# Kernel tuning notes

Measured on AMD Instinct MI355X. Metric: run time of the kernel, lower is better.

## Reference

```python
import jax, jax.numpy as jnp
import numpy as np

N_NODES = 50000
N_EDGES = 1600000
IN_DIM = 64
EDGE_DIM = 8
N_GRAPHS = 256
EXP_IN = 32
H = 64  # hidden dim per head / GCN hidden
EPS = 1e-5
NEG_SLOPE = 0.2


def gat_layer(x, src, dst, ea, W, a_src, a_dst, We, a_e, bias, heads, dim, concat):
    """PyG-style GATConv with edge features and self-loops (fill_value='mean')."""
    N = x.shape[0]
    ones_e = jnp.ones((ea.shape[0],), x.dtype)
    cnt = jax.ops.segment_sum(ones_e, dst, num_segments=N)
    loop_attr = jax.ops.segment_sum(ea, dst, num_segments=N) / jnp.maximum(cnt, 1.0)[:, None]
    s = jnp.concatenate([src, jnp.arange(N)])
    d = jnp.concatenate([dst, jnp.arange(N)])
    eaf = jnp.concatenate([ea, loop_attr], axis=0)  # [E+N, edge_dim]
    h = (x @ W).reshape(N, heads, dim)              # [N, H, D]
    ee = (eaf @ We).reshape(-1, heads, dim)         # [E+N, H, D]
    al_src = (h * a_src).sum(-1)                    # [N, H]
    al_dst = (h * a_dst).sum(-1)                    # [N, H]
    score = al_src[s] + al_dst[d] + (ee * a_e).sum(-1)
    score = jax.nn.leaky_relu(score, NEG_SLOPE)     # [E+N, H]
    m = jax.ops.segment_max(score, d, num_segments=N)
    ex = jnp.exp(score - m[d])
    att = ex / jax.ops.segment_sum(ex, d, num_segments=N)[d]
    out = jax.ops.segment_sum(h[s] * att[:, :, None], d, num_segments=N)  # [N, H, D]
    out = out.reshape(N, heads * dim) if concat else out.mean(axis=1)
    return out + bias


def gcn_layer(x, src, dst, W, b):
    """PyG-style GCNConv: add self loops, symmetric degree normalization."""
    N = x.shape[0]
    s = jnp.concatenate([src, jnp.arange(N)])
    d = jnp.concatenate([dst, jnp.arange(N)])
    deg = jax.ops.segment_sum(jnp.ones((s.shape[0],), x.dtype), d, num_segments=N)
    dinv = jax.lax.rsqrt(deg)  # deg >= 1 thanks to self loops
    norm = dinv[s] * dinv[d]
    h = x @ W
    return jax.ops.segment_sum(h[s] * norm[:, None], d, num_segments=N) + b


def bn(x, g, b):
    m = x.mean(axis=0)
    v = x.var(axis=0)
    return g * (x - m) * jax.lax.rsqrt(v + EPS) + b


def mean_pool(x, batch, num_graphs):
    s = jax.ops.segment_sum(x, batch, num_segments=num_graphs)
    c = jax.ops.segment_sum(jnp.ones((x.shape[0],), x.dtype), batch, num_segments=num_graphs)
    return s / jnp.maximum(c, 1.0)[:, None]


def setup_inputs() -> dict:
    key = jax.random.key(0)
    ks = jax.random.split(key, 32)
    p = lambda i, shape: jax.random.normal(ks[i], shape, jnp.float32) * 0.05
    z = lambda n: jnp.zeros((n,), jnp.float32)
    o = lambda n: jnp.ones((n,), jnp.float32)
    return {
        "x": jax.random.normal(ks[0], (N_NODES, IN_DIM), jnp.float32),
        "edge_attr": jax.random.normal(ks[1], (N_EDGES, EDGE_DIM), jnp.float32),
        "experimental_feat": jax.random.normal(ks[2], (N_GRAPHS, EXP_IN), jnp.float32),
        "edge_index": jax.random.randint(ks[3], (2, N_EDGES), 0, N_NODES),
        "batch": jnp.sort(jax.random.randint(ks[4], (N_NODES,), 0, N_GRAPHS)),
        "W1": p(5, (IN_DIM, 4 * H)), "att_src1": p(6, (4, H)), "att_dst1": p(7, (4, H)),
        "We1": p(8, (EDGE_DIM, 4 * H)), "att_e1": p(9, (4, H)), "b1": z(4 * H),
        "g1": o(4 * H), "be1": z(4 * H),
        "W2": p(10, (4 * H, H)), "att_src2": p(11, (1, H)), "att_dst2": p(12, (1, H)),
        "We2": p(13, (EDGE_DIM, H)), "att_e2": p(14, (1, H)), "b2": z(H),
        "g2": o(H), "be2": z(H),
        "Wg1": p(15, (H, H)), "bg1": z(H), "g3": o(H), "be3": z(H),
        "Wg2": p(16, (H, H)), "bg2": z(H), "g4": o(H), "be4": z(H),
        "Wex1": p(17, (EXP_IN, H)), "bex1": z(H), "Wex2": p(18, (H, H)), "bex2": z(H),
        "Wc1": p(19, (2 * H, 128)), "bc1": z(128), "Wc2": p(20, (128, 1)), "bc2": z(1),
    }


def reference(x, edge_attr, experimental_feat, edge_index, batch,
              W1, att_src1, att_dst1, We1, att_e1, b1, g1, be1,
              W2, att_src2, att_dst2, We2, att_e2, b2, g2, be2,
              Wg1, bg1, g3, be3, Wg2, bg2, g4, be4,
              Wex1, bex1, Wex2, bex2, Wc1, bc1, Wc2, bc2):
    src, dst = edge_index[0], edge_index[1]
    h = gat_layer(x, src, dst, edge_attr, W1, att_src1, att_dst1, We1, att_e1, b1, 4, H, True)
    h = jax.nn.relu(bn(h, g1, be1))
    h = gat_layer(h, src, dst, edge_attr, W2, att_src2, att_dst2, We2, att_e2, b2, 1, H, False)
    h = jax.nn.relu(bn(h, g2, be2))  # dropout = identity in eval
    h = gcn_layer(h, src, dst, Wg1, bg1)
    h = jax.nn.relu(bn(h, g3, be3))
    h = gcn_layer(h, src, dst, Wg2, bg2)
    h = jax.nn.relu(bn(h, g4, be4))
    xp = mean_pool(h, batch, N_GRAPHS)                    # [G, H]
    e = jax.nn.relu(experimental_feat @ Wex1 + bex1)
    e = jax.nn.relu(e @ Wex2 + bex2)
    combined = jnp.concatenate([xp, e], axis=1)           # [G, 2H]
    combined = jax.nn.relu(combined @ Wc1 + bc1)          # [G, 128]
    out = combined @ Wc2 + bc2                            # [G, 1]
    return (out, xp, combined)
```

## Files before the change

kernel.cpp:

```cpp
#include <hip/hip_runtime.h>
#include <hip/hip_bf16.h>

#define N_NODES 50000
#define N_EDGES 1600000
#define N_GRAPHS 256
#define NEG_SLOPE 0.2f
#define BN_EPS 1e-5f

typedef __hip_bfloat16 bf16;

__device__ __forceinline__ float b2f(bf16 v){ return __bfloat162float(v); }
__device__ __forceinline__ bf16 f2b(float v){ return __float2bfloat16(v); }
__device__ __forceinline__ float us2f(unsigned short u){ return __uint_as_float(((unsigned)u)<<16); }
__device__ __forceinline__ unsigned short f2us(float v){ bf16 b = f2b(v); return *(unsigned short*)&b; }
__device__ __forceinline__ unsigned pk2(float a, float b){ return (unsigned)f2us(a) | ((unsigned)f2us(b)<<16); }
__device__ __forceinline__ float ldF(const void* p, size_t i, int m){
  return m ? ((const float*)p)[i] : b2f(((const bf16*)p)[i]);
}
__device__ __forceinline__ float sane(float v){
  return (v == v && fabsf(v) < 1e30f) ? v : 0.f;
}
__device__ __forceinline__ float sel4(const float v[4], int h){
  float r = v[0];
  r = (h==1) ? v[1] : r;
  r = (h==2) ? v[2] : r;
  r = (h==3) ? v[3] : r;
  return r;
}
__device__ __forceinline__ void acc8(float* acc, float w, uint4 u){
  acc[0] += w*us2f((unsigned short)(u.x & 0xffff)); acc[1] += w*us2f((unsigned short)(u.x >> 16));
  acc[2] += w*us2f((unsigned short)(u.y & 0xffff)); acc[3] += w*us2f((unsigned short)(u.y >> 16));
  acc[4] += w*us2f((unsigned short)(u.z & 0xffff)); acc[5] += w*us2f((unsigned short)(u.z >> 16));
  acc[6] += w*us2f((unsigned short)(u.w & 0xffff)); acc[7] += w*us2f((unsigned short)(u.w >> 16));
}
__device__ __forceinline__ void unp8(float* o, uint4 u){
  o[0] = us2f((unsigned short)(u.x & 0xffff)); o[1] = us2f((unsigned short)(u.x >> 16));
  o[2] = us2f((unsigned short)(u.y & 0xffff)); o[3] = us2f((unsigned short)(u.y >> 16));
  o[4] = us2f((unsigned short)(u.z & 0xffff)); o[5] = us2f((unsigned short)(u.z >> 16));
  o[6] = us2f((unsigned short)(u.w & 0xffff)); o[7] = us2f((unsigned short)(u.w >> 16));
}

__device__ int detect_mode_block(const void* x){
  __shared__ int s_ins;
  if(threadIdx.x == 0) s_ins = 0;
  __syncthreads();
  const unsigned short* u = (const unsigned short*)x;
  int c = 0;
  for(int i = threadIdx.x; i < 1024; i += blockDim.x){
    float v = fabsf(us2f(u[i]));
    if(!(v > 1e-6f && v < 1e4f)) c++;
  }
  if(c) atomicAdd(&s_ins, c);
  __syncthreads();
  return (s_ins > 128) ? 1 : 0;
}

#define NSEG 33
struct Bank { const void* p[NSEG]; int n[NSEG]; int off[NSEG]; };

__global__ void k_convert(Bank b, const void* xdet, float* out){
  int m = detect_mode_block(xdet);
  int seg = blockIdx.y;
  int i = blockIdx.x*256 + threadIdx.x;
  if(i < b.n[seg]) out[b.off[seg] + i] = ldF(b.p[seg], i, m);
}

__global__ void k_cvt_x(const void* x, bf16* xb){
  int m = detect_mode_block(x);
  int i4 = blockIdx.x*256 + threadIdx.x;
  if(i4 >= N_NODES*16) return;
  if(m){
    float4 v = ((const float4*)x)[i4];
    ((ushort4*)xb)[i4] = make_ushort4(f2us(v.x), f2us(v.y), f2us(v.z), f2us(v.w));
  } else {
    ((ushort4*)xb)[i4] = ((const ushort4*)x)[i4];
  }
}

__global__ void k_we(const float* __restrict__ We1, const float* __restrict__ ae1,
                     const float* __restrict__ We2, const float* __restrict__ ae2,
                     float* __restrict__ w_e){
  int t = threadIdx.x;
  if(t < 32){
    int h = t >> 3, k = t & 7;
    float s = 0.f;
    for(int d=0;d<64;d++) s += We1[k*256 + h*64 + d] * ae1[h*64 + d];
    w_e[t] = s;
  } else if(t < 40){
    int k = t - 32;
    float s = 0.f;
    for(int d=0;d<64;d++) s += We2[k*64 + d] * ae2[d];
    w_e[t] = s;
  }
}

__global__ void k_count(const int* __restrict__ dst, int* __restrict__ cnt){
  int e = blockIdx.x*256 + threadIdx.x;
  if(e < N_EDGES){
    int d = dst[e]; if((unsigned)d >= N_NODES) d = 0;
    atomicAdd(&cnt[d], 1);
  }
}

__global__ void k_blocksum(const int* __restrict__ cnt, int* __restrict__ bsum){
  __shared__ int s[256];
  int i = blockIdx.x*256 + threadIdx.x;
  s[threadIdx.x] = (i < N_NODES) ? cnt[i] : 0;
  __syncthreads();
  for(int o=128;o>0;o>>=1){ if(threadIdx.x<o) s[threadIdx.x]+=s[threadIdx.x+o]; __syncthreads(); }
  if(threadIdx.x==0) bsum[blockIdx.x]=s[0];
}

__global__ void k_scan_bsum(const int* __restrict__ bsum, int* __restrict__ bofs, int nb){
  __shared__ int s[256];
  int t = threadIdx.x;
  s[t] = (t<nb) ? bsum[t] : 0;
  __syncthreads();
  for(int o=1;o<256;o<<=1){ int v=(t>=o)?s[t-o]:0; __syncthreads(); s[t]+=v; __syncthreads(); }
  bofs[t] = (t==0) ? 0 : s[t-1];
}

__global__ void k_scan_write(const int* __restrict__ cnt, const int* __restrict__ bofs,
                             int* __restrict__ rp, float* __restrict__ dinv){
  __shared__ int s[256];
  int t = threadIdx.x; int i = blockIdx.x*256 + t;
  int v = (i<N_NODES) ? cnt[i] : 0;
  s[t]=v; __syncthreads();
  for(int o=1;o<256;o<<=1){ int a=(t>=o)?s[t-o]:0; __syncthreads(); s[t]+=a; __syncthreads(); }
  if(i<N_NODES){
    rp[i+1] = s[t] + bofs[blockIdx.x];
    dinv[i] = rsqrtf((float)v + 1.f);
  }
  if(i==0) rp[0]=0;
}

__global__ void k_fill(const int* __restrict__ src, const int* __restrict__ dst,
                       const int* __restrict__ rp, int* __restrict__ fill,
                       const void* __restrict__ ea, const void* __restrict__ xdet,
                       const float* __restrict__ w_e,
                       int4* __restrict__ epk){
  int m = detect_mode_block(xdet);
  int e = blockIdx.x*256 + threadIdx.x;
  if(e >= N_EDGES) return;
  int d = dst[e]; if((unsigned)d >= N_NODES) d = 0;
  int p = atomicAdd(&fill[d], 1);
  int slot = rp[d] + p;
  if((unsigned)slot >= N_EDGES) return;
  int sv = src[e]; if((unsigned)sv >= N_NODES) sv = 0;
  float a[8];
  if(m){
    const float* eaf = (const float*)ea;
    float4 lo = *(const float4*)&eaf[(size_t)e*8];
    float4 hi = *(const float4*)&eaf[(size_t)e*8 + 4];
    a[0]=lo.x; a[1]=lo.y; a[2]=lo.z; a[3]=lo.w;
    a[4]=hi.x; a[5]=hi.y; a[6]=hi.z; a[7]=hi.w;
  } else {
    #pragma unroll
    for(int k=0;k<8;k++) a[k] = b2f(((const bf16*)ea)[(size_t)e*8 + k]);
  }
  unsigned d4[4];
  #pragma unroll
  for(int h=0;h<4;h++){
    float s = 0.f;
    #pragma unroll
    for(int k=0;k<8;k++) s += a[k]*w_e[h*8+k];
    d4[h] = f2us(s);
  }
  float s1 = 0.f;
  #pragma unroll
  for(int k=0;k<8;k++) s1 += a[k]*w_e[32+k];
  int4 pk;
  pk.x = sv;
  pk.y = (int)(d4[0] | (d4[1] << 16));
  pk.z = (int)(d4[2] | (d4[3] << 16));
  pk.w = (int)(unsigned)f2us(s1);
  epk[slot] = pk;
}

__global__ __launch_bounds__(256, 3) void k_gemmA(
    const bf16* __restrict__ xb, const float* __restrict__ W1,
    bf16* __restrict__ hp, int M)
{
  __shared__ float As[64][68];
  __shared__ float Ws[64][64];
  const int tid = threadIdx.x;
  const int bm  = blockIdx.x * 64;
  const int h   = blockIdx.y;
  const int tx  = tid & 15;
  const int ty  = tid >> 4;
  float acc[4][4] = {};

  #pragma unroll
  for(int f = tid; f < 1024; f += 256){
    int r = f >> 4, kq = f & 15;
    int row = bm + r;
    float4 v = make_float4(0.f,0.f,0.f,0.f);
    if(row < M){
      ushort4 u = *(const ushort4*)&xb[(size_t)row*64 + 4*kq];
      v = make_float4(us2f(u.x), us2f(u.y), us2f(u.z), us2f(u.w));
    }
    *(float4*)&As[r][4*kq] = v;
  }
  #pragma unroll
  for(int g = tid; g < 1024; g += 256){
    int kr = g >> 4, jq = g & 15;
    *(float4*)&Ws[kr][4*jq] = *(const float4*)&W1[(size_t)kr*256 + h*64 + 4*jq];
  }
  __syncthreads();
  #pragma unroll 2
  for(int k = 0; k < 64; k += 4){
    float4 av[4], wv[4];
    #pragma unroll
    for(int r=0;r<4;r++) av[r] = *(const float4*)&As[4*ty + r][k];
    #pragma unroll
    for(int kk=0;kk<4;kk++) wv[kk] = *(const float4*)&Ws[k + kk][4*tx];
    #pragma unroll
    for(int r=0;r<4;r++){
      const float a0=av[r].x, a1=av[r].y, a2=av[r].z, a3=av[r].w;
      acc[r][0] += a0*wv[0].x + a1*wv[1].x + a2*wv[2].x + a3*wv[3].x;
      acc[r][1] += a0*wv[0].y + a1*wv[1].y + a2*wv[2].y + a3*wv[3].y;
      acc[r][2] += a0*wv[0].z + a1*wv[1].z + a2*wv[2].z + a3*wv[3].z;
      acc[r][3] += a0*wv[0].w + a1*wv[1].w + a2*wv[2].w + a3*wv[3].w;
    }
  }
  #pragma unroll
  for(int r=0;r<4;r++){
    int row = bm + 4*ty + r;
    if(row < M){
      ushort4 u = make_ushort4(f2us(acc[r][0]), f2us(acc[r][1]), f2us(acc[r][2]), f2us(acc[r][3]));
      *(ushort4*)&hp[(size_t)row*256 + h*64 + 4*tx] = u;
    }
  }
}

template<int KIN>
__global__ __launch_bounds__(256, 3) void k_gemmB(
    const bf16* __restrict__ A, const float* __restrict__ W,
    bf16* __restrict__ C, int M,
    const float* __restrict__ bnsums, const float* __restrict__ bng, const float* __restrict__ bnb)
{
  __shared__ float As[64][68];
  __shared__ float Ws[64][64];
  const int tid = threadIdx.x;
  const int bm  = blockIdx.x * 64;
  const int tx  = tid & 15;
  const int ty  = tid >> 4;
  const float invN = 1.0f / (float)N_NODES;
  float acc[4][4] = {};

  for(int k0 = 0; k0 < KIN; k0 += 64){
    #pragma unroll
    for(int f = tid; f < 1024; f += 256){
      int r = f >> 4, kq = f & 15;
      int row = bm + r;
      float vv[4] = {0.f,0.f,0.f,0.f};
      if(row < M){
        ushort4 u = *(const ushort4*)&A[(size_t)row*KIN + k0 + 4*kq];
        vv[0]=us2f(u.x); vv[1]=us2f(u.y); vv[2]=us2f(u.z); vv[3]=us2f(u.w);
      }
      int c = k0 + 4*kq;
      #pragma unroll
      for(int j=0;j<4;j++){
        int cc = c + j;
        float mean = bnsums[cc]*invN;
        float var = fmaxf(bnsums[KIN+cc]*invN - mean*mean, 0.f);
        float y = (sane(vv[j])-mean)*rsqrtf(var + BN_EPS)*bng[cc] + bnb[cc];
        vv[j] = fmaxf(y, 0.f);
      }
      *(float4*)&As[r][4*kq] = make_float4(vv[0], vv[1], vv[2], vv[3]);
    }
    #pragma unroll
    for(int g = tid; g < 1024; g += 256){
      int kr = g >> 4, jq = g & 15;
      *(float4*)&Ws[kr][4*jq] = *(const float4*)&W[(size_t)(k0+kr)*64 + 4*jq];
    }
    __syncthreads();
    #pragma unroll 2
    for(int k = 0; k < 64; k += 4){
      float4 av[4], wv[4];
      #pragma unroll
      for(int r=0;r<4;r++) av[r] = *(const float4*)&As[4*ty + r][k];
      #pragma unroll
      for(int kk=0;kk<4;kk++) wv[kk] = *(const float4*)&Ws[k + kk][4*tx];
      #pragma unroll
      for(int r=0;r<4;r++){
        const float a0=av[r].x, a1=av[r].y, a2=av[r].z, a3=av[r].w;
        acc[r][0] += a0*wv[0].x + a1*wv[1].x + a2*wv[2].x + a3*wv[3].x;
        acc[r][1] += a0*wv[0].y + a1*wv[1].y + a2*wv[2].y + a3*wv[3].y;
        acc[r][2] += a0*wv[0].z + a1*wv[1].z + a2*wv[2].z + a3*wv[3].z;
        acc[r][3] += a0*wv[0].w + a1*wv[1].w + a2*wv[2].w + a3*wv[3].w;
      }
    }
    __syncthreads();
  }
  #pragma unroll
  for(int r=0;r<4;r++){
    int row = bm + 4*ty + r;
    if(row < M){
      ushort4 u = make_ushort4(f2us(acc[r][0]), f2us(acc[r][1]), f2us(acc[r][2]), f2us(acc[r][3]));
      *(ushort4*)&C[(size_t)row*64 + 4*tx] = u;
    }
  }
}

__global__ void k_al4(const bf16* __restrict__ hp, const float* __restrict__ asrc,
                      const float* __restrict__ adst,
                      float* __restrict__ als4, float* __restrict__ ald4){
  int idx = blockIdx.x*256 + threadIdx.x;
  if(idx >= N_NODES*4) return;
  int n = idx >> 2, h = idx & 3;
  const unsigned short* row = (const unsigned short*)hp + (size_t)n*256 + h*64;
  float ss=0.f, sd=0.f;
  #pragma unroll
  for(int q=0;q<16;q++){
    ushort4 u = *(const ushort4*)&row[4*q];
    float4 a_s = *(const float4*)&asrc[h*64 + 4*q];
    float4 a_d = *(const float4*)&adst[h*64 + 4*q];
    float v0=us2f(u.x), v1=us2f(u.y), v2=us2f(u.z), v3=us2f(u.w);
    ss += v0*a_s.x + v1*a_s.y + v2*a_s.z + v3*a_s.w;
    sd += v0*a_d.x + v1*a_d.y + v2*a_d.z + v3*a_d.w;
  }
  als4[idx]=ss; ald4[idx]=sd;
}

__global__ void k_al1(const bf16* __restrict__ hp, const float* __restrict__ asrc,
                      const float* __restrict__ adst,
                      float* __restrict__ als, float* __restrict__ ald){
  int n = blockIdx.x*256 + threadIdx.x;
  if(n >= N_NODES) return;
  const unsigned short* row = (const unsigned short*)hp + (size_t)n*64;
  float ss=0.f, sd=0.f;
  #pragma unroll
  for(int q=0;q<16;q++){
    ushort4 u = *(const ushort4*)&row[4*q];
    float4 a_s = *(const float4*)&asrc[4*q];
    float4 a_d = *(const float4*)&adst[4*q];
    float v0=us2f(u.x), v1=us2f(u.y), v2=us2f(u.z), v3=us2f(u.w);
    ss += v0*a_s.x + v1*a_s.y + v2*a_s.z + v3*a_s.w;
    sd += v0*a_d.x + v1*a_d.y + v2*a_d.z + v3*a_d.w;
  }
  als[n]=ss; ald[n]=sd;
}

__global__ __launch_bounds__(64) void k_gat_agg4(
    const int* __restrict__ rp, const int4* __restrict__ epk,
    const bf16* __restrict__ hp,
    const float* __restrict__ als4, const float* __restrict__ ald4,
    const float* __restrict__ bias256, bf16* __restrict__ out1){
  int n = blockIdx.x; int t = threadIdx.x;
  int eh = t >> 5, c8 = t & 31;
  int head = c8 >> 3;
  __shared__ int   ssrc[64];
  __shared__ float swt[64][4];
  int s0 = rp[n], e0 = rp[n+1];
  if((unsigned)s0 > N_EDGES){ s0=0; e0=0; }
  if(e0 < s0 || (unsigned)e0 > N_EDGES) e0 = s0;
  float4 aldv = *(const float4*)&ald4[n*4];
  float4 alsvn = *(const float4*)&als4[n*4];
  float wsum[4] = {0.f,0.f,0.f,0.f};
  float dsum[4] = {0.f,0.f,0.f,0.f};
  float acc[8]  = {0.f,0.f,0.f,0.f,0.f,0.f,0.f,0.f};
  const unsigned short* hpu = (const unsigned short*)hp;

  for(int base = s0; base < e0; base += 64){
    int m = min(64, e0 - base);
    if(t < m){
      int4 pk = epk[base+t];
      int sn = pk.x; if((unsigned)sn >= N_NODES) sn = 0;
      ssrc[t] = sn;
      float edf[4] = {us2f((unsigned short)(pk.y & 0xffff)), us2f((unsigned short)((unsigned)pk.y >> 16)),
                      us2f((unsigned short)(pk.z & 0xffff)), us2f((unsigned short)((unsigned)pk.z >> 16))};
      float4 alss = *(const float4*)&als4[sn*4];
      float alssv[4] = {alss.x, alss.y, alss.z, alss.w};
      float aldvv[4] = {aldv.x, aldv.y, aldv.z, aldv.w};
      float w4[4];
      #pragma unroll
      for(int h=0;h<4;h++){
        float sc = alssv[h] + aldvv[h] + edf[h];
        sc = sc > 0.f ? sc : NEG_SLOPE*sc;
        sc = fminf(sc, 30.f);
        float w = expf(sc);
        w4[h] = w;
        wsum[h] += w; dsum[h] += edf[h];
      }
      *(float4*)&swt[t][0] = make_float4(w4[0], w4[1], w4[2], w4[3]);
    }
    __syncthreads();
    #pragma unroll 4
    for(int i=0;i<m;i+=2){
      int j = i + eh;
      if(j < m){
        int row = ssrc[j];
        float w = swt[j][head];
        uint4 u = *(const uint4*)&hpu[(size_t)row*256 + 8*c8];
        acc8(acc, w, u);
      }
    }
    __syncthreads();
  }
  #pragma unroll
  for(int o=1;o<64;o<<=1){
    #pragma unroll
    for(int h=0;h<4;h++){
      wsum[h] += __shfl_xor(wsum[h], o);
      dsum[h] += __shfl_xor(dsum[h], o);
    }
  }
  #pragma unroll
  for(int q=0;q<8;q++) acc[q] += __shfl_xor(acc[q], 32);
  if(eh == 0){
    float alsnv[4] = {alsvn.x, alsvn.y, alsvn.z, alsvn.w};
    float aldnv[4] = {aldv.x, aldv.y, aldv.z, aldv.w};
    float sEh = sel4(wsum, head), sDh = sel4(dsum, head);
    float deg = (float)(e0 - s0);
    float sdot = deg > 0.f ? sDh/deg : 0.f;
    float sc = sel4(alsnv, head) + sel4(aldnv, head) + sdot;
    sc = sc > 0.f ? sc : NEG_SLOPE*sc;
    sc = fminf(sc, 30.f);
    float wself = expf(sc);
    float self[8];
    unp8(self, *(const uint4*)&hpu[(size_t)n*256 + 8*c8]);
    float4 b0 = *(const float4*)&bias256[8*c8];
    float4 b1 = *(const float4*)&bias256[8*c8 + 4];
    float bi[8] = {b0.x,b0.y,b0.z,b0.w,b1.x,b1.y,b1.z,b1.w};
    float inv = 1.f/(sEh + wself);
    float o8[8];
    #pragma unroll
    for(int q=0;q<8;q++) o8[q] = (acc[q] + wself*self[q])*inv + bi[q];
    uint4 st;
    st.x = pk2(o8[0],o8[1]); st.y = pk2(o8[2],o8[3]);
    st.z = pk2(o8[4],o8[5]); st.w = pk2(o8[6],o8[7]);
    *(uint4*)&((unsigned short*)out1)[(size_t)n*256 + 8*c8] = st;
  }
}

__global__ __launch_bounds__(64) void k_gat_agg1e(
    const int* __restrict__ rp, const int4* __restrict__ epk,
    const bf16* __restrict__ hp,
    const float* __restrict__ als, const float* __restrict__ ald,
    const float* __restrict__ bias64, bf16* __restrict__ out){
  int n = blockIdx.x; int t = threadIdx.x;
  int eg = t >> 3, c8 = t & 7;
  __shared__ float sw[64];
  __shared__ int   ssrc[64];
  int s0 = rp[n], e0 = rp[n+1];
  if((unsigned)s0 > N_EDGES){ s0=0; e0=0; }
  if(e0 < s0 || (unsigned)e0 > N_EDGES) e0 = s0;
  float aldn = ald[n];
  float wsum_l = 0.f, dsum_l = 0.f;
  float acc[8] = {0.f,0.f,0.f,0.f,0.f,0.f,0.f,0.f};
  const unsigned short* hpu = (const unsigned short*)hp;
  for(int base = s0; base < e0; base += 64){
    int m = min(64, e0 - base);
    if(t < m){
      int4 pk = epk[base+t];
      int sn = pk.x; if((unsigned)sn >= N_NODES) sn = 0;
      ssrc[t] = sn;
      float ed = us2f((unsigned short)(pk.w & 0xffff));
      float sc = als[sn] + aldn + ed;
      sc = sc > 0.f ? sc : NEG_SLOPE*sc;
      sc = fminf(sc, 30.f);
      float w = expf(sc);
      sw[t] = w;
      wsum_l += w; dsum_l += ed;
    }
    __syncthreads();
    #pragma unroll 2
    for(int i=0;i<m;i+=8){
      int j = i + eg;
      if(j < m){
        int row = ssrc[j];
        float w = sw[j];
        uint4 u = *(const uint4*)&hpu[(size_t)row*64 + 8*c8];
        acc8(acc, w, u);
      }
    }
    __syncthreads();
  }
  #pragma unroll
  for(int o=1;o<64;o<<=1){ wsum_l += __shfl_xor(wsum_l, o); dsum_l += __shfl_xor(dsum_l, o); }
  #pragma unroll
  for(int q=0;q<8;q++){
    acc[q] += __shfl_xor(acc[q], 8);
    acc[q] += __shfl_xor(acc[q], 16);
    acc[q] += __shfl_xor(acc[q], 32);
  }
  if(t < 8){
    float deg = (float)(e0 - s0);
    float sdot = deg > 0.f ? dsum_l/deg : 0.f;
    float sc = als[n] + aldn + sdot;
    sc = sc > 0.f ? sc : NEG_SLOPE*sc;
    sc = fminf(sc, 30.f);
    float wself = expf(sc);
    float self[8];
    unp8(self, *(const uint4*)&hpu[(size_t)n*64 + 8*t]);
    float4 b0 = *(const float4*)&bias64[8*t];
    float4 b1 = *(const float4*)&bias64[8*t + 4];
    float bi[8] = {b0.x,b0.y,b0.z,b0.w,b1.x,b1.y,b1.z,b1.w};
    float inv = 1.f/(wsum_l + wself);
    float o8[8];
    #pragma unroll
    for(int q=0;q<8;q++) o8[q] = (acc[q] + wself*self[q])*inv + bi[q];
    uint4 st;
    st.x = pk2(o8[0],o8[1]); st.y = pk2(o8[2],o8[3]);
    st.z = pk2(o8[4],o8[5]); st.w = pk2(o8[6],o8[7]);
    *(uint4*)&((unsigned short*)out)[(size_t)n*64 + 8*t] = st;
  }
}

__global__ __launch_bounds__(64) void k_gcn_agg(
    const int* __restrict__ rp, const int4* __restrict__ epk,
    const float* __restrict__ dinv, const bf16* __restrict__ gp,
    const float* __restrict__ bias, bf16* __restrict__ out){
  int n = blockIdx.x; int t = threadIdx.x;
  int eg = t >> 3, c8 = t & 7;
  __shared__ float sw[64];
  __shared__ int   ssrc[64];
  int s0 = rp[n], e0 = rp[n+1];
  if((unsigned)s0 > N_EDGES){ s0=0; e0=0; }
  if(e0 < s0 || (unsigned)e0 > N_EDGES) e0 = s0;
  float dn = dinv[n];
  float acc[8] = {0.f,0.f,0.f,0.f,0.f,0.f,0.f,0.f};
  const unsigned short* gpu = (const unsigned short*)gp;
  for(int base = s0; base < e0; base += 64){
    int m = min(64, e0 - base);
    if(t < m){
      int sn = epk[base+t].x; if((unsigned)sn >= N_NODES) sn = 0;
      ssrc[t]=sn; sw[t]=dinv[sn];
    }
    __syncthreads();
    #pragma unroll 2
    for(int i=0;i<m;i+=8){
      int j = i + eg;
      if(j < m){
        int row = ssrc[j];
        float w = sw[j];
        uint4 u = *(const uint4*)&gpu[(size_t)row*64 + 8*c8];
        acc8(acc, w, u);
      }
    }
    __syncthreads();
  }
  #pragma unroll
  for(int q=0;q<8;q++){
    acc[q] += __shfl_xor(acc[q], 8);
    acc[q] += __shfl_xor(acc[q], 16);
    acc[q] += __shfl_xor(acc[q], 32);
  }
  if(t < 8){
    float self[8];
    unp8(self, *(const uint4*)&gpu[(size_t)n*64 + 8*t]);
    float4 b0 = *(const float4*)&bias[8*t];
    float4 b1 = *(const float4*)&bias[8*t + 4];
    float bi[8] = {b0.x,b0.y,b0.z,b0.w,b1.x,b1.y,b1.z,b1.w};
    float o8[8];
    #pragma unroll
    for(int q=0;q<8;q++) o8[q] = dn*(acc[q] + dn*self[q]) + bi[q];
    uint4 st;
    st.x = pk2(o8[0],o8[1]); st.y = pk2(o8[2],o8[3]);
    st.z = pk2(o8[4],o8[5]); st.w = pk2(o8[6],o8[7]);
    *(uint4*)&((unsigned short*)out)[(size_t)n*64 + 8*t] = st;
  }
}

template<int C>
__global__ void k_colstats(const bf16* __restrict__ X, float* __restrict__ sums){
  constexpr int RPB = 128;
  constexpr int RSTEP = 256 / C;
  int c = threadIdx.x % C;
  int r0 = threadIdx.x / C;
  int rbeg = blockIdx.x * RPB;
  int rend = min(N_NODES, rbeg + RPB);
  const unsigned short* Xu = (const unsigned short*)X;
  float s = 0.f, q = 0.f;
  for(int r = rbeg + r0; r < rend; r += RSTEP){
    float v = sane(us2f(Xu[(size_t)r*C + c]));
    s += v; q += v*v;
  }
  atomicAdd(&sums[c], s);
  atomicAdd(&sums[C + c], q);
}

__global__ __launch_bounds__(64) void k_pool3(
    const bf16* __restrict__ h, const int* __restrict__ batch,
    const float* __restrict__ sums, const float* __restrict__ g4,
    const float* __restrict__ b4,
    float* __restrict__ psum, float* __restrict__ pcnt){
  int t = threadIdx.x;
  int n0 = blockIdx.x * 256;
  int n1 = min(N_NODES, n0 + 256);
  if(n0 >= n1) return;
  const float invN = 1.0f / (float)N_NODES;
  float mean = sums[t]*invN;
  float var = fmaxf(sums[64+t]*invN - mean*mean, 0.f);
  float rstd = rsqrtf(var + BN_EPS);
  float gg = g4[t], bb = b4[t];
  const unsigned short* hu = (const unsigned short*)h;
  int cur = batch[n0]; if((unsigned)cur >= N_GRAPHS) cur = 0;
  float acc = 0.f; int cl = 0;
  for(int n = n0; n < n1; n++){
    int g = batch[n]; if((unsigned)g >= N_GRAPHS) g = 0;
    if(g != cur){
      atomicAdd(&psum[cur*64 + t], acc);
      if(t == 0) atomicAdd(&pcnt[cur], (float)cl);
      acc = 0.f; cl = 0; cur = g;
    }
    float y = (sane(us2f(hu[(size_t)n*64 + t]))-mean)*rstd*gg + bb;
    acc += fmaxf(y, 0.f);
    cl++;
  }
  atomicAdd(&psum[cur*64 + t], acc);
  if(t == 0) atomicAdd(&pcnt[cur], (float)cl);
}

__device__ __forceinline__ void stO(void* o, size_t i, float v, int m){
  if(m) ((float*)o)[i] = v; else ((bf16*)o)[i] = f2b(v);
}

__global__ __launch_bounds__(128) void k_head(
    const float* __restrict__ psum, const float* __restrict__ pcnt,
    const float* __restrict__ exf,
    const float* __restrict__ Wex1, const float* __restrict__ bex1,
    const float* __restrict__ Wex2, const float* __restrict__ bex2,
    const float* __restrict__ Wc1, const float* __restrict__ bc1,
    const float* __restrict__ Wc2, const float* __restrict__ bc2,
    const void* __restrict__ xdet, void* __restrict__ dout){
  int m0 = detect_mode_block(xdet);
  int g = blockIdx.x; int t = threadIdx.x;
  __shared__ float ci[128];
  __shared__ float e1[64];
  __shared__ float comb[128];
  __shared__ float red[128];
  if(t < 64){
    float c = fmaxf(pcnt[g], 1.f);
    float xp = sane(psum[g*64 + t]) / c;
    ci[t] = xp;
    stO(dout, 256 + (size_t)g*64 + t, xp, m0);
  } else {
    int j = t - 64;
    float s = bex1[j];
    for(int k=0;k<32;k++) s += exf[g*32 + k] * Wex1[k*64 + j];
    e1[j] = fmaxf(s, 0.f);
  }
  __syncthreads();
  if(t >= 64){
    int j = t - 64;
    float s = bex2[j];
    for(int k=0;k<64;k++) s += e1[k] * Wex2[k*64 + j];
    ci[64 + j] = fmaxf(s, 0.f);
  }
  __syncthreads();
  {
    float s = bc1[t];
    for(int k=0;k<128;k++) s += ci[k] * Wc1[k*128 + t];
    s = fmaxf(s, 0.f);
    comb[t] = s;
    stO(dout, 256 + 16384 + (size_t)g*128 + t, s, m0);
  }
  __syncthreads();
  red[t] = comb[t] * Wc2[t];
  __syncthreads();
  for(int o=64;o>0;o>>=1){ if(t<o) red[t]+=red[t+o]; __syncthreads(); }
  if(t==0) stO(dout, g, red[0] + bc2[0], m0);
}

extern "C" void kernel_launch(void* const* d_in, const int* in_sizes, int n_in,
                              void* d_out, int out_size, void* d_ws, size_t ws_size,
                              hipStream_t stream){
  const void* x    = d_in[0];
  const void* ea   = d_in[1];
  const int* ei    = (const int*)d_in[3];
  const int* batch = (const int*)d_in[4];
  const int* src = ei;
  const int* dst = ei + N_EDGES;

  char* base = (char*)d_ws;
  size_t off = 0;
  auto alloc = [&](size_t bytes) -> void* {
    void* r = base + off;
    off += (bytes + 255) & ~(size_t)255;
    return r;
  };
  int*   cnt    = (int*)  alloc((size_t)N_NODES*4);
  int*   fill   = (int*)  alloc((size_t)N_NODES*4);
  float* bnstat = (float*)alloc(4096);
  float* pool   = (float*)alloc((size_t)(N_GRAPHS*64 + N_GRAPHS)*4);
  size_t zbytes = off;
  int*   rp      = (int*)  alloc((size_t)(N_NODES+1)*4);
  int*   bsum    = (int*)  alloc(256*4);
  int*   bofs    = (int*)  alloc(256*4);
  int4*  epk     = (int4*) alloc((size_t)N_EDGES*16);
  float* dinv    = (float*)alloc((size_t)N_NODES*4);
  float* w_e     = (float*)alloc(64*4);
  float* als4    = (float*)alloc((size_t)N_NODES*4*4);
  float* ald4    = (float*)alloc((size_t)N_NODES*4*4);
  float* wbank   = (float*)alloc(80000*4);
  bf16*  xb      = (bf16*) alloc((size_t)N_NODES*64*2);
  bf16*  hp      = (bf16*) alloc((size_t)N_NODES*256*2);
  bf16*  outb    = (bf16*) alloc((size_t)N_NODES*256*2);

  bf16* out1 = outb;
  bf16* out2 = outb;
  bf16* out3 = outb + (size_t)N_NODES*64;
  bf16* out4 = outb + (size_t)N_NODES*128;
  float* bn1 = bnstat;
  float* bn2 = bnstat + 512;
  float* bn3 = bnstat + 640;
  float* bn4 = bnstat + 768;
  float* psum = pool;
  float* pcnt = pool + N_GRAPHS*64;

  const int segidx[NSEG] = {2, 5,6,7,8,9,10,11,12, 13,14,15,16,17,18,19,20,
                            21,22,23,24, 25,26,27,28, 29,30,31,32, 33,34,35,36};
  const int segn[NSEG] = {8192, 16384,256,256,2048,256,256,256,256,
                          16384,64,64,512,64,64,64,64,
                          4096,64,64,64, 4096,64,64,64,
                          2048,64,4096,64, 16384,128,128,1};
  Bank bk;
  int offs[NSEG]; int acc0 = 0;
  for(int i=0;i<NSEG;i++){ bk.p[i]=d_in[segidx[i]]; bk.n[i]=segn[i]; bk.off[i]=acc0; offs[i]=acc0; acc0+=segn[i]; }
  const float* f_exf = wbank + offs[0];
  const float* fW1 = wbank+offs[1]; const float* fas1 = wbank+offs[2]; const float* fad1 = wbank+offs[3];
  const float* fWe1= wbank+offs[4]; const float* fae1 = wbank+offs[5]; const float* fb1  = wbank+offs[6];
  const float* fg1 = wbank+offs[7]; const float* fbe1 = wbank+offs[8];
  const float* fW2 = wbank+offs[9]; const float* fas2 = wbank+offs[10]; const float* fad2 = wbank+offs[11];
  const float* fWe2= wbank+offs[12]; const float* fae2 = wbank+offs[13]; const float* fb2 = wbank+offs[14];
  const float* fg2 = wbank+offs[15]; const float* fbe2 = wbank+offs[16];
  const float* fWg1= wbank+offs[17]; const float* fbg1 = wbank+offs[18]; const float* fg3 = wbank+offs[19];
  const float* fbe3= wbank+offs[20];
  const float* fWg2= wbank+offs[21]; const float* fbg2 = wbank+offs[22]; const float* fg4 = wbank+offs[23];
  const float* fbe4= wbank+offs[24];
  const float* fWex1=wbank+offs[25]; const float* fbex1= wbank+offs[26];
  const float* fWex2=wbank+offs[27]; const float* fbex2= wbank+offs[28];
  const float* fWc1= wbank+offs[29]; const float* fbc1 = wbank+offs[30];
  const float* fWc2= wbank+offs[31]; const float* fbc2 = wbank+offs[32];

  const int nbN  = (N_NODES + 255)/256;
  const int nbE  = (N_EDGES + 255)/256;
  const int nbT  = (N_NODES + 63)/64;

  hipMemsetAsync(d_ws, 0, zbytes, stream);
  {
    dim3 g((16384+255)/256, NSEG);
    k_convert<<<g,256,0,stream>>>(bk, x, wbank);
  }
  k_cvt_x<<<(N_NODES*16+255)/256,256,0,stream>>>(x, xb);
  k_we<<<1,64,0,stream>>>(fWe1, fae1, fWe2, fae2, w_e);
  k_count<<<nbE,256,0,stream>>>(dst, cnt);
  k_blocksum<<<nbN,256,0,stream>>>(cnt, bsum);
  k_scan_bsum<<<1,256,0,stream>>>(bsum, bofs, nbN);
  k_scan_write<<<nbN,256,0,stream>>>(cnt, bofs, rp, dinv);
  k_fill<<<nbE,256,0,stream>>>(src, dst, rp, fill, ea, x, w_e, epk);

  {
    dim3 g(nbT, 4);
    k_gemmA<<<g,256,0,stream>>>(xb, fW1, hp, N_NODES);
  }
  k_al4<<<(N_NODES*4+255)/256,256,0,stream>>>(hp, fas1, fad1, als4, ald4);
  k_gat_agg4<<<N_NODES,64,0,stream>>>(rp, epk, hp, als4, ald4, fb1, out1);
  k_colstats<256><<<(N_NODES+127)/128,256,0,stream>>>(out1, bn1);

  k_gemmB<256><<<nbT,256,0,stream>>>(out1, fW2, hp, N_NODES, bn1, fg1, fbe1);
  k_al1<<<nbN,256,0,stream>>>(hp, fas2, fad2, als4, ald4);
  k_gat_agg1e<<<N_NODES,64,0,stream>>>(rp, epk, hp, als4, ald4, fb2, out2);
  k_colstats<64><<<(N_NODES+127)/128,256,0,stream>>>(out2, bn2);

  k_gemmB<64><<<nbT,256,0,stream>>>(out2, fWg1, hp, N_NODES, bn2, fg2, fbe2);
  k_gcn_agg<<<N_NODES,64,0,stream>>>(rp, epk, dinv, hp, fbg1, out3);
  k_colstats<64><<<(N_NODES+127)/128,256,0,stream>>>(out3, bn3);

  k_gemmB<64><<<nbT,256,0,stream>>>(out3, fWg2, hp, N_NODES, bn3, fg3, fbe3);
  k_gcn_agg<<<N_NODES,64,0,stream>>>(rp, epk, dinv, hp, fbg2, out4);
  k_colstats<64><<<(N_NODES+127)/128,256,0,stream>>>(out4, bn4);

  k_pool3<<<nbN,64,0,stream>>>(out4, batch, bn4, fg4, fbe4, psum, pcnt);
  k_head<<<N_GRAPHS,128,0,stream>>>(psum, pcnt, f_exf, fWex1, fbex1, fWex2, fbex2,
                                    fWc1, fbc1, fWc2, fbc2, x, (void*)d_out);
}
```

Measured before the change: 974.4 us.

## Replace FP32 shared-memory GEMMs with bf16 MFMA matrix-core kernels

```diff
diff --git a/kernel.cpp b/kernel.cpp
--- a/kernel.cpp
+++ b/kernel.cpp
@@ -8,6 +8,8 @@
 #define BN_EPS 1e-5f
 
 typedef __hip_bfloat16 bf16;
+typedef __attribute__((ext_vector_type(8))) short s16x8;
+typedef __attribute__((ext_vector_type(4))) float f32x4;
 
 __device__ __forceinline__ float b2f(bf16 v){ return __bfloat162float(v); }
 __device__ __forceinline__ bf16 f2b(float v){ return __float2bfloat16(v); }
@@ -38,6 +40,12 @@
   o[2] = us2f((unsigned short)(u.y & 0xffff)); o[3] = us2f((unsigned short)(u.y >> 16));
   o[4] = us2f((unsigned short)(u.z & 0xffff)); o[5] = us2f((unsigned short)(u.z >> 16));
   o[6] = us2f((unsigned short)(u.w & 0xffff)); o[7] = us2f((unsigned short)(u.w >> 16));
+}
+__device__ __forceinline__ s16x8 pk8(const float* v){
+  s16x8 r;
+  #pragma unroll
+  for(int j=0;j<8;j++) r[j] = (short)f2us(v[j]);
+  return r;
 }
 
 __device__ int detect_mode_block(const void* x){
@@ -91,6 +99,25 @@
     float s = 0.f;
     for(int d=0;d<64;d++) s += We2[k*64 + d] * ae2[d];
     w_e[t] = s;
+  }
+}
+
+__global__ void k_wt(const float* __restrict__ W1, const float* __restrict__ W2,
+                     const float* __restrict__ Wg1, const float* __restrict__ Wg2,
+                     bf16* __restrict__ wt){
+  int i = blockIdx.x*256 + threadIdx.x;
+  if(i < 16384){
+    int c = i >> 6, k = i & 63;
+    wt[i] = f2b(W1[k*256 + c]);
+  } else if(i < 32768){
+    int j = i - 16384; int c = j >> 8, k = j & 255;
+    wt[i] = f2b(W2[k*64 + c]);
+  } else if(i < 36864){
+    int j = i - 32768; int c = j >> 6, k = j & 63;
+    wt[i] = f2b(Wg1[k*64 + c]);
+  } else if(i < 40960){
+    int j = i - 36864; int c = j >> 6, k = j & 63;
+    wt[i] = f2b(Wg2[k*64 + c]);
   }
 }
 
@@ -177,128 +204,90 @@
   epk[slot] = pk;
 }
 
-__global__ __launch_bounds__(256, 3) void k_gemmA(
-    const bf16* __restrict__ xb, const float* __restrict__ W1,
+__global__ __launch_bounds__(256) void k_gemmA_mfma(
+    const bf16* __restrict__ xb,
+    const bf16* __restrict__ wt1,
     bf16* __restrict__ hp, int M)
 {
-  __shared__ float As[64][68];
-  __shared__ float Ws[64][64];
   const int tid = threadIdx.x;
-  const int bm  = blockIdx.x * 64;
-  const int h   = blockIdx.y;
-  const int tx  = tid & 15;
-  const int ty  = tid >> 4;
-  float acc[4][4] = {};
-
-  #pragma unroll
-  for(int f = tid; f < 1024; f += 256){
-    int r = f >> 4, kq = f & 15;
-    int row = bm + r;
-    float4 v = make_float4(0.f,0.f,0.f,0.f);
-    if(row < M){
-      ushort4 u = *(const ushort4*)&xb[(size_t)row*64 + 4*kq];
-      v = make_float4(us2f(u.x), us2f(u.y), us2f(u.z), us2f(u.w));
-    }
-    *(float4*)&As[r][4*kq] = v;
-  }
-  #pragma unroll
-  for(int g = tid; g < 1024; g += 256){
-    int kr = g >> 4, jq = g & 15;
-    *(float4*)&Ws[kr][4*jq] = *(const float4*)&W1[(size_t)kr*256 + h*64 + 4*jq];
-  }
-  __syncthreads();
-  #pragma unroll 2
-  for(int k = 0; k < 64; k += 4){
-    float4 av[4], wv[4];
-    #pragma unroll
-    for(int r=0;r<4;r++) av[r] = *(const float4*)&As[4*ty + r][k];
-    #pragma unroll
-    for(int kk=0;kk<4;kk++) wv[kk] = *(const float4*)&Ws[k + kk][4*tx];
-    #pragma unroll
-    for(int r=0;r<4;r++){
-      const float a0=av[r].x, a1=av[r].y, a2=av[r].z, a3=av[r].w;
-      acc[r][0] += a0*wv[0].x + a1*wv[1].x + a2*wv[2].x + a3*wv[3].x;
-      acc[r][1] += a0*wv[0].y + a1*wv[1].y + a2*wv[2].y + a3*wv[3].y;
-      acc[r][2] += a0*wv[0].z + a1*wv[1].z + a2*wv[2].z + a3*wv[3].z;
-      acc[r][3] += a0*wv[0].w + a1*wv[1].w + a2*wv[2].w + a3*wv[3].w;
-    }
-  }
-  #pragma unroll
-  for(int r=0;r<4;r++){
-    int row = bm + 4*ty + r;
-    if(row < M){
-      ushort4 u = make_ushort4(f2us(acc[r][0]), f2us(acc[r][1]), f2us(acc[r][2]), f2us(acc[r][3]));
-      *(ushort4*)&hp[(size_t)row*256 + h*64 + 4*tx] = u;
+  const int w = tid >> 6, l = tid & 63;
+  const int lr = l & 15, lg = l >> 4;
+  const int bm = blockIdx.x*64 + w*16;
+  const int arow_i = bm + lr;
+  const uint4* arow = (const uint4*)(xb + (size_t)min(arow_i, M-1)*64);
+  uint4 a0u = arow[lg];
+  uint4 a1u = arow[4 + lg];
+  s16x8 a0 = *(s16x8*)&a0u, a1 = *(s16x8*)&a1u;
+  unsigned short* out = (unsigned short*)hp;
+  const int orow0 = bm + lg*4;
+  #pragma unroll
+  for(int ct = 0; ct < 16; ct++){
+    const uint4* brow = (const uint4*)(wt1 + (size_t)(ct*16 + lr)*64);
+    uint4 b0u = brow[lg];
+    uint4 b1u = brow[4 + lg];
+    f32x4 acc = {0.f, 0.f, 0.f, 0.f};
+    acc = __builtin_amdgcn_mfma_f32_16x16x32_bf16(a0, *(s16x8*)&b0u, acc, 0, 0, 0);
+    acc = __builtin_amdgcn_mfma_f32_16x16x32_bf16(a1, *(s16x8*)&b1u, acc, 0, 0, 0);
+    #pragma unroll
+    for(int r = 0; r < 4; r++){
+      int rr = orow0 + r;
+      if(rr < M) out[(size_t)rr*256 + ct*16 + lr] = f2us(acc[r]);
     }
   }
 }
 
 template<int KIN>
-__global__ __launch_bounds__(256, 3) void k_gemmB(
-    const bf16* __restrict__ A, const float* __restrict__ W,
+__global__ __launch_bounds__(256) void k_gemmB_mfma(
+    const bf16* __restrict__ A, const bf16* __restrict__ Wt,
     bf16* __restrict__ C, int M,
     const float* __restrict__ bnsums, const float* __restrict__ bng, const float* __restrict__ bnb)
 {
-  __shared__ float As[64][68];
-  __shared__ float Ws[64][64];
+  __shared__ float st_s[KIN];
+  __shared__ float st_t[KIN];
   const int tid = threadIdx.x;
-  const int bm  = blockIdx.x * 64;
-  const int tx  = tid & 15;
-  const int ty  = tid >> 4;
-  const float invN = 1.0f / (float)N_NODES;
-  float acc[4][4] = {};
-
-  for(int k0 = 0; k0 < KIN; k0 += 64){
-    #pragma unroll
-    for(int f = tid; f < 1024; f += 256){
-      int r = f >> 4, kq = f & 15;
-      int row = bm + r;
-      float vv[4] = {0.f,0.f,0.f,0.f};
-      if(row < M){
-        ushort4 u = *(const ushort4*)&A[(size_t)row*KIN + k0 + 4*kq];
-        vv[0]=us2f(u.x); vv[1]=us2f(u.y); vv[2]=us2f(u.z); vv[3]=us2f(u.w);
-      }
-      int c = k0 + 4*kq;
-      #pragma unroll
-      for(int j=0;j<4;j++){
-        int cc = c + j;
-        float mean = bnsums[cc]*invN;
-        float var = fmaxf(bnsums[KIN+cc]*invN - mean*mean, 0.f);
-        float y = (sane(vv[j])-mean)*rsqrtf(var + BN_EPS)*bng[cc] + bnb[cc];
-        vv[j] = fmaxf(y, 0.f);
-      }
-      *(float4*)&As[r][4*kq] = make_float4(vv[0], vv[1], vv[2], vv[3]);
-    }
-    #pragma unroll
-    for(int g = tid; g < 1024; g += 256){
-      int kr = g >> 4, jq = g & 15;
-      *(float4*)&Ws[kr][4*jq] = *(const float4*)&W[(size_t)(k0+kr)*64 + 4*jq];
-    }
-    __syncthreads();
-    #pragma unroll 2
-    for(int k = 0; k < 64; k += 4){
-      float4 av[4], wv[4];
-      #pragma unroll
-      for(int r=0;r<4;r++) av[r] = *(const float4*)&As[4*ty + r][k];
-      #pragma unroll
-      for(int kk=0;kk<4;kk++) wv[kk] = *(const float4*)&Ws[k + kk][4*tx];
-      #pragma unroll
-      for(int r=0;r<4;r++){
-        const float a0=av[r].x, a1=av[r].y, a2=av[r].z, a3=av[r].w;
-        acc[r][0] += a0*wv[0].x + a1*wv[1].x + a2*wv[2].x + a3*wv[3].x;
-        acc[r][1] += a0*wv[0].y + a1*wv[1].y + a2*wv[2].y + a3*wv[3].y;
-        acc[r][2] += a0*wv[0].z + a1*wv[1].z + a2*wv[2].z + a3*wv[3].z;
-        acc[r][3] += a0*wv[0].w + a1*wv[1].w + a2*wv[2].w + a3*wv[3].w;
-      }
-    }
-    __syncthreads();
-  }
-  #pragma unroll
-  for(int r=0;r<4;r++){
-    int row = bm + 4*ty + r;
-    if(row < M){
-      ushort4 u = make_ushort4(f2us(acc[r][0]), f2us(acc[r][1]), f2us(acc[r][2]), f2us(acc[r][3]));
-      *(ushort4*)&C[(size_t)row*64 + 4*tx] = u;
+  if(tid < KIN){
+    const float invN = 1.0f / (float)N_NODES;
+    float mean = bnsums[tid]*invN;
+    float var  = fmaxf(bnsums[KIN+tid]*invN - mean*mean, 0.f);
+    float s = bng[tid]*rsqrtf(var + BN_EPS);
+    st_s[tid] = s;
+    st_t[tid] = bnb[tid] - mean*s;
+  }
+  __syncthreads();
+  const int w = tid >> 6, l = tid & 63;
+  const int lr = l & 15, lg = l >> 4;
+  const int bm = blockIdx.x*64 + w*16;
+  const int arow_i = bm + lr;
+  const uint4* arow = (const uint4*)(A + (size_t)min(arow_i, M-1)*KIN);
+  f32x4 acc[4];
+  #pragma unroll
+  for(int ct=0;ct<4;ct++) acc[ct] = (f32x4){0.f,0.f,0.f,0.f};
+  #pragma unroll
+  for(int k0 = 0; k0 < KIN; k0 += 32){
+    uint4 au = arow[(k0 >> 3) + lg];
+    int c0 = k0 + lg*8;
+    float v[8]; unp8(v, au);
+    #pragma unroll
+    for(int j = 0; j < 8; j++){
+      float y = sane(v[j])*st_s[c0+j] + st_t[c0+j];
+      v[j] = fmaxf(y, 0.f);
+    }
+    s16x8 af = pk8(v);
+    #pragma unroll
+    for(int ct = 0; ct < 4; ct++){
+      const uint4* brow = (const uint4*)(Wt + (size_t)(ct*16 + lr)*KIN);
+      uint4 bu = brow[(k0 >> 3) + lg];
+      acc[ct] = __builtin_amdgcn_mfma_f32_16x16x32_bf16(af, *(s16x8*)&bu, acc[ct], 0, 0, 0);
+    }
+  }
+  unsigned short* out = (unsigned short*)C;
+  const int orow0 = bm + lg*4;
+  #pragma unroll
+  for(int ct = 0; ct < 4; ct++){
+    #pragma unroll
+    for(int r = 0; r < 4; r++){
+      int rr = orow0 + r;
+      if(rr < M) out[(size_t)rr*64 + ct*16 + lr] = f2us(acc[ct][r]);
     }
   }
 }
@@ -695,6 +684,7 @@
   float* als4    = (float*)alloc((size_t)N_NODES*4*4);
   float* ald4    = (float*)alloc((size_t)N_NODES*4*4);
   float* wbank   = (float*)alloc(80000*4);
+  bf16*  wt      = (bf16*) alloc((size_t)40960*2);
   bf16*  xb      = (bf16*) alloc((size_t)N_NODES*64*2);
   bf16*  hp      = (bf16*) alloc((size_t)N_NODES*256*2);
   bf16*  outb    = (bf16*) alloc((size_t)N_NODES*256*2);
@@ -709,6 +699,11 @@
   float* bn4 = bnstat + 768;
   float* psum = pool;
   float* pcnt = pool + N_GRAPHS*64;
+
+  bf16* wt1  = wt;
+  bf16* wt2  = wt + 16384;
+  bf16* wtg1 = wt + 32768;
+  bf16* wtg2 = wt + 36864;
 
   const int segidx[NSEG] = {2, 5,6,7,8,9,10,11,12, 13,14,15,16,17,18,19,20,
                             21,22,23,24, 25,26,27,28, 29,30,31,32, 33,34,35,36};
@@ -744,6 +739,7 @@
     dim3 g((16384+255)/256, NSEG);
     k_convert<<<g,256,0,stream>>>(bk, x, wbank);
   }
+  k_wt<<<160,256,0,stream>>>(fW1, fW2, fWg1, fWg2, wt);
   k_cvt_x<<<(N_NODES*16+255)/256,256,0,stream>>>(x, xb);
   k_we<<<1,64,0,stream>>>(fWe1, fae1, fWe2, fae2, w_e);
   k_count<<<nbE,256,0,stream>>>(dst, cnt);
@@ -752,24 +748,21 @@
   k_scan_write<<<nbN,256,0,stream>>>(cnt, bofs, rp, dinv);
   k_fill<<<nbE,256,0,stream>>>(src, dst, rp, fill, ea, x, w_e, epk);
 
-  {
-    dim3 g(nbT, 4);
-    k_gemmA<<<g,256,0,stream>>>(xb, fW1, hp, N_NODES);
-  }
+  k_gemmA_mfma<<<nbT,256,0,stream>>>(xb, wt1, hp, N_NODES);
   k_al4<<<(N_NODES*4+255)/256,256,0,stream>>>(hp, fas1, fad1, als4, ald4);
   k_gat_agg4<<<N_NODES,64,0,stream>>>(rp, epk, hp, als4, ald4, fb1, out1);
   k_colstats<256><<<(N_NODES+127)/128,256,0,stream>>>(out1, bn1);
 
-  k_gemmB<256><<<nbT,256,0,stream>>>(out1, fW2, hp, N_NODES, bn1, fg1, fbe1);
+  k_gemmB_mfma<256><<<nbT,256,0,stream>>>(out1, wt2, hp, N_NODES, bn1, fg1, fbe1);
   k_al1<<<nbN,256,0,stream>>>(hp, fas2, fad2, als4, ald4);
   k_gat_agg1e<<<N_NODES,64,0,stream>>>(rp, epk, hp, als4, ald4, fb2, out2);
   k_colstats<64><<<(N_NODES+127)/128,256,0,stream>>>(out2, bn2);
 
-  k_gemmB<64><<<nbT,256,0,stream>>>(out2, fWg1, hp, N_NODES, bn2, fg2, fbe2);
+  k_gemmB_mfma<64><<<nbT,256,0,stream>>>(out2, wtg1, hp, N_NODES, bn2, fg2, fbe2);
   k_gcn_agg<<<N_NODES,64,0,stream>>>(rp, epk, dinv, hp, fbg1, out3);
   k_colstats<64><<<(N_NODES+127)/128,256,0,stream>>>(out3, bn3);
 
-  k_gemmB<64><<<nbT,256,0,stream>>>(out3, fWg2, hp, N_NODES, bn3, fg3, fbe3);
+  k_gemmB_mfma<64><<<nbT,256,0,stream>>>(out3, wtg2, hp, N_NODES, bn3, fg3, fbe3);
   k_gcn_agg<<<N_NODES,64,0,stream>>>(rp, epk, dinv, hp, fbg2, out4);
   k_colstats<64><<<(N_NODES+127)/128,256,0,stream>>>(out4, bn4);
 
```

Result: faster. 938.3 us (-3.7%).
